# Kernel tuning notes

Hardware: AMD Instinct MI355X
Metric: run time of the kernel (lower is better)

## Reference

```python
import jax, jax.numpy as jnp
import numpy as np

NUM_POS_FEATS = 16
TEMPERATURE = 10000.0
SCALE = 100.0

def sine_pos_embed(x):
    # x: [..., 1] -> [..., NUM_POS_FEATS], interleaved sin/cos per torch get_sine_pos_embed
    i = jnp.arange(NUM_POS_FEATS, dtype=jnp.float32)
    dim_t = TEMPERATURE ** (2.0 * jnp.floor(i / 2.0) / NUM_POS_FEATS)
    emb = x * SCALE / dim_t  # [..., NUM_POS_FEATS]
    s = jnp.sin(emb[..., 0::2])
    c = jnp.cos(emb[..., 1::2])
    return jnp.stack([s, c], axis=-1).reshape(emb.shape)

def setup_inputs() -> dict:
    key = jax.random.key(0)
    ks = jax.random.split(key, 6)
    B, N, D, V, H = 4, 900, 256, 16, 8
    queries = jax.random.normal(ks[0], (B, N, D), jnp.float32)
    current_ref_points = jax.random.uniform(ks[1], (B, N, 4), dtype=jnp.float32)
    prev_ref_points = jax.random.uniform(ks[2], (B, N, 4), dtype=jnp.float32)
    vote_w = jax.random.normal(ks[3], (V * 2, D), jnp.float32) * (1.0 / np.sqrt(D))
    vote_b = jnp.zeros((V * 2,), jnp.float32)
    proj_w = jax.random.normal(ks[4], (H, NUM_POS_FEATS), jnp.float32) * 0.25
    proj_b = jnp.zeros((H,), jnp.float32)
    return {"queries": queries, "current_ref_points": current_ref_points,
            "prev_ref_points": prev_ref_points, "vote_w": vote_w, "vote_b": vote_b,
            "proj_w": proj_w, "proj_b": proj_b}

def reference(queries, current_ref_points, prev_ref_points, vote_w, vote_b, proj_w, proj_b):
    B, N, D = queries.shape
    V = vote_w.shape[0] // 2
    # vote_generator: MLP with num_layers=1 == single Linear
    votes = (queries @ vote_w.T + vote_b).reshape(B, N, V, 2)
    vote_pos = current_ref_points[:, :, None, :2] + votes  # [B,N,V,2]
    centers = current_ref_points[:, :, :2]                  # [B,N,2]
    vf = vote_pos.reshape(B, N * V, 2)
    # squared euclidean distances [B, N*V, N] (cdist then **2)
    d2 = (jnp.sum(vf ** 2, -1)[:, :, None]
          + jnp.sum(centers ** 2, -1)[:, None, :]
          - 2.0 * jnp.einsum('bik,bjk->bij', vf, centers))
    d2 = jnp.maximum(d2, 0.0)
    sigma = jnp.mean(current_ref_points[:, :, 2:], -1, keepdims=True) / 2.0  # [B,N,1]
    sigma_flat = jnp.tile(sigma, (1, V, 1))  # faithful to torch .repeat(1,V,1)
    scores = jnp.exp(-d2 / (2.0 * sigma_flat ** 2))          # [B,N*V,N]
    imap = scores.reshape(B, N, V, N).sum(2)                  # vote-sum -> [B,N,N]
    imap = imap / jnp.maximum(jnp.sum(jnp.abs(imap), 2, keepdims=True), 1e-12)  # F.normalize p=1
    imap = 1.0 - imap
    pos = sine_pos_embed(imap[..., None])                     # [B,N,N,16]
    # pos_proj: 1x1 conv (bias) + ReLU over channel dim
    out = jnp.einsum('bnmf,hf->bhnm', pos, proj_w) + proj_b[None, :, None, None]
    return jax.nn.relu(out)
```

## Files before the change

### kernel.cpp

```cpp
#include <hip/hip_runtime.h>

#define NPF 16
#define NH 8
#define NV 16
#define NN 900
#define ND 256
#define NB 4

__global__ __launch_bounds__(256)
__attribute__((amdgpu_waves_per_eu(4, 4)))
void hough_fused(
    const float* __restrict__ queries,
    const float* __restrict__ cur_ref,
    const float* __restrict__ vote_w,
    const float* __restrict__ vote_b,
    const float* __restrict__ proj_w,
    const float* __restrict__ proj_b,
    float* __restrict__ out)
{
    __shared__ __align__(16) float qs[ND];
    __shared__ float part[256];
    __shared__ float vp[NV * 2];
    __shared__ float s2i[NV];
    __shared__ __align__(16) float4 sCoef[NV];
    __shared__ float red[4];
    __shared__ float s_inv;

    const int tid = threadIdx.x;
    const int bn  = blockIdx.x;
    const int b   = bn / NN;
    const int n   = bn - b * NN;

    qs[tid] = queries[(size_t)bn * ND + tid];
    __syncthreads();

    {
        const int o     = tid & 31;
        const int chunk = tid >> 5;
        const float4* wv = (const float4*)(vote_w + o * ND + chunk * 32);
        const float4* qv = (const float4*)(qs + chunk * 32);
        float p = 0.f;
#pragma unroll
        for (int j = 0; j < 8; j++) {
            float4 w4 = wv[j];
            float4 q4 = qv[j];
            p += w4.x * q4.x + w4.y * q4.y + w4.z * q4.z + w4.w * q4.w;
        }
        part[tid] = p;
    }
    __syncthreads();

    if (tid < 32) {
        float s = vote_b[tid];
#pragma unroll
        for (int c = 0; c < 8; c++) s += part[c * 32 + tid];
        vp[tid] = s + cur_ref[((size_t)b * NN + n) * 4 + (tid & 1)];
    } else if (tid >= 64 && tid < 64 + NV) {
        int v = tid - 64;
        int j = (n * NV + v) % NN;
        float c2 = cur_ref[((size_t)b * NN + j) * 4 + 2];
        float c3 = cur_ref[((size_t)b * NN + j) * 4 + 3];
        float sg = (c2 + c3) * 0.25f;
        s2i[v] = 0.5f / (sg * sg);
    }
    __syncthreads();

    if (tid < NV) {
        float x  = vp[2 * tid];
        float y  = vp[2 * tid + 1];
        float s2 = s2i[tid];
        sCoef[tid] = make_float4(2.f * s2 * x, 2.f * s2 * y,
                                 -s2 * (x * x + y * y), -s2);
    }
    __syncthreads();

    float acc[4] = {0.f, 0.f, 0.f, 0.f};
    const float4* cr4 = (const float4*)cur_ref + (size_t)b * NN;

#pragma unroll 1
    for (int c = 0; c < 2; c++) {
        float ax[8], ay[8], c0[8], ns[8];
#pragma unroll
        for (int v = 0; v < 8; v++) {
            float4 f = sCoef[c * 8 + v];
            ax[v] = f.x; ay[v] = f.y; c0[v] = f.z; ns[v] = f.w;
        }
#pragma unroll
        for (int i = 0; i < 4; i++) {
            int m = tid + 256 * i;
            if (m < NN) {
                float4 cr = cr4[m];
                float cx = cr.x, cy = cr.y;
                float cc = cx * cx + cy * cy;
                float a = 0.f;
#pragma unroll
                for (int v = 0; v < 8; v++) {
                    float t = fmaf(ax[v], cx, c0[v]);
                    t = fmaf(ay[v], cy, t);
                    t = fmaf(ns[v], cc, t);
                    a += __expf(fminf(t, 0.f));
                }
                acc[i] += a;
            }
        }
    }

    float lsum = acc[0] + acc[1] + acc[2] + acc[3];
#pragma unroll
    for (int off = 32; off > 0; off >>= 1) lsum += __shfl_down(lsum, off, 64);
    if ((tid & 63) == 0) red[tid >> 6] = lsum;
    __syncthreads();
    if (tid == 0)
        s_inv = 1.0f / fmaxf(red[0] + red[1] + red[2] + red[3], 1e-12f);
    __syncthreads();
    const float inv = s_inv;

    float xv[4];
#pragma unroll
    for (int i = 0; i < 4; i++) xv[i] = 1.0f - acc[i] * inv;

    const float invt[8] = {100.0f, 31.622776601683793f, 10.0f, 3.1622776601683795f,
                           1.0f, 0.31622776601683794f, 0.1f, 0.031622776601683791f};

    float* outbase = out + (((size_t)(b * NH) * NN + n) * NN);

#pragma unroll 1
    for (int pass = 0; pass < 2; pass++) {
        float Wr[64];
#pragma unroll
        for (int k = 0; k < 64; k++) Wr[k] = proj_w[pass * 64 + k];
        float Pb[4];
#pragma unroll
        for (int h = 0; h < 4; h++) Pb[h] = proj_b[pass * 4 + h];

        float* opass = outbase + (size_t)pass * 4 * NN * NN;

#pragma unroll
        for (int i = 0; i < 4; i++) {
            int m = tid + 256 * i;
            if (m < NN) {
                float x = xv[i];
                float sk[8], ck[8];
#pragma unroll
                for (int k = 0; k < 8; k++) {
                    float a = x * invt[k];
                    sk[k] = __sinf(a);
                    ck[k] = __cosf(a);
                }
                float* op = opass + m;
#pragma unroll
                for (int h = 0; h < 4; h++) {
                    float o = Pb[h];
#pragma unroll
                    for (int k = 0; k < 8; k++) {
                        o = fmaf(Wr[h * 16 + 2 * k],     sk[k], o);
                        o = fmaf(Wr[h * 16 + 2 * k + 1], ck[k], o);
                    }
                    op[(size_t)h * NN * NN] = fmaxf(o, 0.f);
                }
            }
        }
    }
}

extern "C" void kernel_launch(void* const* d_in, const int* in_sizes, int n_in,
                              void* d_out, int out_size, void* d_ws, size_t ws_size,
                              hipStream_t stream) {
    const float* queries = (const float*)d_in[0];
    const float* cur_ref = (const float*)d_in[1];
    const float* vote_w  = (const float*)d_in[3];
    const float* vote_b  = (const float*)d_in[4];
    const float* proj_w  = (const float*)d_in[5];
    const float* proj_b  = (const float*)d_in[6];
    float* out = (float*)d_out;

    hough_fused<<<NB * NN, 256, 0, stream>>>(queries, cur_ref, vote_w, vote_b,
                                             proj_w, proj_b, out);
}
```

Before: 151.2 us.

## Replace per-element sin/cos projection with interpolated shared-memory lookup table

A small pre-kernel tabulates the 8-head projected sine embedding (bias, weights, sin/cos) at 513 points over x in [0,1] into workspace. The main kernel loads this table into shared memory and evaluates each output by linear interpolation, replacing 16 transcendentals and 128 FMAs per element. The Gaussian vote scores now use exp2 with log2(e) folded into the coefficients. This trades exactness for an approximation error of roughly bin width squared times the highest frequency, and adds 32KB of shared memory per block plus an extra launch.

```diff
diff --git a/kernel.cpp b/kernel.cpp
--- a/kernel.cpp
+++ b/kernel.cpp
@@ -6,16 +6,41 @@
 #define NN 900
 #define ND 256
 #define NB 4
+#define NM (NN * NN)
+#define NBINS 512
+#define LOG2E 1.44269504088896340736f
 
-__global__ __launch_bounds__(256)
-__attribute__((amdgpu_waves_per_eu(4, 4)))
-void hough_fused(
+__global__ __launch_bounds__(256) void hough_lut(
+    const float* __restrict__ proj_w,
+    const float* __restrict__ proj_b,
+    float2* __restrict__ lut)
+{
+    const float invt[8] = {100.0f, 31.622776601683793f, 10.0f, 3.1622776601683795f,
+                           1.0f, 0.31622776601683794f, 0.1f, 0.031622776601683791f};
+    for (int i = threadIdx.x; i < NH * NBINS; i += 256) {
+        int h   = i / NBINS;
+        int bin = i - h * NBINS;
+        float x0 = (float)bin * (1.0f / NBINS);
+        float x1 = (float)(bin + 1) * (1.0f / NBINS);
+        float g0 = proj_b[h], g1 = proj_b[h];
+#pragma unroll
+        for (int k = 0; k < 8; k++) {
+            float ws = proj_w[h * NPF + 2 * k];
+            float wc = proj_w[h * NPF + 2 * k + 1];
+            float a0 = x0 * invt[k], a1 = x1 * invt[k];
+            g0 = fmaf(ws, __sinf(a0), fmaf(wc, __cosf(a0), g0));
+            g1 = fmaf(ws, __sinf(a1), fmaf(wc, __cosf(a1), g1));
+        }
+        lut[i] = make_float2(g0, g1 - g0);
+    }
+}
+
+__global__ __launch_bounds__(256) void hough_fused(
     const float* __restrict__ queries,
     const float* __restrict__ cur_ref,
     const float* __restrict__ vote_w,
     const float* __restrict__ vote_b,
-    const float* __restrict__ proj_w,
-    const float* __restrict__ proj_b,
+    const float2* __restrict__ lut,
     float* __restrict__ out)
 {
     __shared__ __align__(16) float qs[ND];
@@ -25,12 +50,16 @@
     __shared__ __align__(16) float4 sCoef[NV];
     __shared__ float red[4];
     __shared__ float s_inv;
+    __shared__ __align__(16) float2 sLut[NH * NBINS];
 
     const int tid = threadIdx.x;
     const int bn  = blockIdx.x;
     const int b   = bn / NN;
     const int n   = bn - b * NN;
 
+#pragma unroll
+    for (int j = 0; j < 8; j++)
+        ((float4*)sLut)[tid + 256 * j] = ((const float4*)lut)[tid + 256 * j];
     qs[tid] = queries[(size_t)bn * ND + tid];
     __syncthreads();
 
@@ -68,7 +97,7 @@
     if (tid < NV) {
         float x  = vp[2 * tid];
         float y  = vp[2 * tid + 1];
-        float s2 = s2i[tid];
+        float s2 = s2i[tid] * LOG2E;
         sCoef[tid] = make_float4(2.f * s2 * x, 2.f * s2 * y,
                                  -s2 * (x * x + y * y), -s2);
     }
@@ -98,7 +127,7 @@
                     float t = fmaf(ax[v], cx, c0[v]);
                     t = fmaf(ay[v], cy, t);
                     t = fmaf(ns[v], cc, t);
-                    a += __expf(fminf(t, 0.f));
+                    a += exp2f(fminf(t, 0.f));
                 }
                 acc[i] += a;
             }
@@ -115,49 +144,20 @@
     __syncthreads();
     const float inv = s_inv;
 
-    float xv[4];
+    float* outrow = out + ((size_t)(b * NH) * NN + n) * NN;
 #pragma unroll
-    for (int i = 0; i < 4; i++) xv[i] = 1.0f - acc[i] * inv;
-
-    const float invt[8] = {100.0f, 31.622776601683793f, 10.0f, 3.1622776601683795f,
-                           1.0f, 0.31622776601683794f, 0.1f, 0.031622776601683791f};
-
-    float* outbase = out + (((size_t)(b * NH) * NN + n) * NN);
-
-#pragma unroll 1
-    for (int pass = 0; pass < 2; pass++) {
-        float Wr[64];
+    for (int i = 0; i < 4; i++) {
+        int m = tid + 256 * i;
+        if (m < NN) {
+            float x = 1.0f - acc[i] * inv;
+            float t = fminf(fmaxf(x * (float)NBINS, 0.f), (float)NBINS - 0.001f);
+            int   ib = (int)t;
+            float fr = t - (float)ib;
+            float* op = outrow + m;
 #pragma unroll
-        for (int k = 0; k < 64; k++) Wr[k] = proj_w[pass * 64 + k];
-        float Pb[4];
-#pragma unroll
-        for (int h = 0; h < 4; h++) Pb[h] = proj_b[pass * 4 + h];
-
-        float* opass = outbase + (size_t)pass * 4 * NN * NN;
-
-#pragma unroll
-        for (int i = 0; i < 4; i++) {
-            int m = tid + 256 * i;
-            if (m < NN) {
-                float x = xv[i];
-                float sk[8], ck[8];
-#pragma unroll
-                for (int k = 0; k < 8; k++) {
-                    float a = x * invt[k];
-                    sk[k] = __sinf(a);
-                    ck[k] = __cosf(a);
-                }
-                float* op = opass + m;
-#pragma unroll
-                for (int h = 0; h < 4; h++) {
-                    float o = Pb[h];
-#pragma unroll
-                    for (int k = 0; k < 8; k++) {
-                        o = fmaf(Wr[h * 16 + 2 * k],     sk[k], o);
-                        o = fmaf(Wr[h * 16 + 2 * k + 1], ck[k], o);
-                    }
-                    op[(size_t)h * NN * NN] = fmaxf(o, 0.f);
-                }
+            for (int h = 0; h < NH; h++) {
+                float2 vs = sLut[h * NBINS + ib];
+                op[(size_t)h * NM] = fmaxf(fmaf(vs.y, fr, vs.x), 0.f);
             }
         }
     }
@@ -173,7 +173,9 @@
     const float* proj_w  = (const float*)d_in[5];
     const float* proj_b  = (const float*)d_in[6];
     float* out = (float*)d_out;
+    float2* lut = (float2*)d_ws;
 
+    hough_lut<<<1, 256, 0, stream>>>(proj_w, proj_b, lut);
     hough_fused<<<NB * NN, 256, 0, stream>>>(queries, cur_ref, vote_w, vote_b,
-                                             proj_w, proj_b, out);
+                                             lut, out);
 }
```

Measured after the change: 157.5 us. +4.2%, slower.
